# Kernel tuning notes

Hardware: AMD Instinct MI355X
Metric: run time of the kernel (lower is better)

## Reference

```python
import jax, jax.numpy as jnp
import numpy as np

E, K, H, I = 16, 4, 2048, 1024
B, S = 1, 2048


def setup_inputs() -> dict:
    key = jax.random.key(0)
    ks = jax.random.split(key, 5)
    scale_in = 1.0 / np.sqrt(H)
    scale_mid = 1.0 / np.sqrt(I)
    return {
        "x": jax.random.normal(ks[0], (B, S, H), dtype=jnp.float32),
        "gate_w": jax.random.normal(ks[1], (E, H), dtype=jnp.float32) * scale_in,
        "w1_gate": jax.random.normal(ks[2], (E, I, H), dtype=jnp.float32) * scale_in,
        "w1_up": jax.random.normal(ks[3], (E, I, H), dtype=jnp.float32) * scale_in,
        "w2": jax.random.normal(ks[4], (E, H, I), dtype=jnp.float32) * scale_mid,
        "topk": K,
    }


def reference(x, gate_w, w1_gate, w1_up, w2, topk):
    orig_shape = x.shape
    xt = x.reshape(-1, x.shape[-1])            # [T, H]
    T = xt.shape[0]
    n_exp = gate_w.shape[0]

    # Router: top-k logits, softmax over the selected k (as in the torch code).
    logits = xt @ gate_w.T                      # [T, E]
    topk_vals, topk_ids = jax.lax.top_k(logits, topk)
    topk_w = jax.nn.softmax(topk_vals, axis=-1)  # [T, K]

    # Dense per-token-per-expert combine weight; 0 for unselected experts.
    # Mathematically identical to the gather/scatter-add loop: unselected
    # experts contribute expert_out * 0.
    gate_dense = jnp.zeros((T, n_exp), dtype=xt.dtype)
    gate_dense = gate_dense.at[jnp.arange(T)[:, None], topk_ids].add(topk_w)

    # SwiGLU per expert (dense over experts; weights zero-out unused ones).
    g = jnp.einsum("th,eih->tei", xt, w1_gate)   # [T, E, I]
    u = jnp.einsum("th,eih->tei", xt, w1_up)     # [T, E, I]
    h = jax.nn.silu(g) * u                        # [T, E, I]
    out = jnp.einsum("tei,te,ehi->th", h, gate_dense, w2)  # [T, H]
    return out.reshape(orig_shape)
```

## Files before the change

### kernel.cpp

```cpp
#include <hip/hip_runtime.h>
#include <hip/hip_bf16.h>
#include <stdint.h>

#define NEXP 16
#define KSEL 4
#define HDIM 2048
#define IDIM 1024
#define TTOK 2048
#define MAXTILES 80
#define NTA 8
#define NTB 16
#define MAXBA (MAXTILES * NTA)
#define MAXBB (MAXTILES * NTB)

typedef __attribute__((ext_vector_type(8))) short bf16x8;
typedef __attribute__((ext_vector_type(4))) float f32x4;
typedef unsigned int u32;

__device__ __forceinline__ uint32_t pack2(float a, float b) {
  __hip_bfloat162 h = __float22bfloat162_rn(float2{a, b});
  uint32_t u;
  __builtin_memcpy(&u, &h, 4);
  return u;
}
__device__ __forceinline__ ushort bf1(float a) {
  __hip_bfloat16 h = __float2bfloat16(a);
  ushort u;
  __builtin_memcpy(&u, &h, 2);
  return u;
}
__device__ __forceinline__ float bf2f(ushort u) {
  uint32_t v = (uint32_t)u << 16;
  float f;
  __builtin_memcpy(&f, &v, 4);
  return f;
}
__device__ __forceinline__ void gload16(const ushort* g, ushort* l) {
  __builtin_amdgcn_global_load_lds(
      (const __attribute__((address_space(1))) u32*)g,
      (__attribute__((address_space(3))) u32*)l, 16, 0, 0);
}
__device__ __forceinline__ int swzread(int row, int q) {
  return row * 32 + ((q ^ ((row >> 1) & 3)) << 3);
}

__global__ __launch_bounds__(256) void cvtw_kernel(
    const float* __restrict__ src, ushort* __restrict__ dst, int n8)
{
  const int stride = gridDim.x * 256;
  for (int i = blockIdx.x * 256 + threadIdx.x; i < n8; i += stride) {
    float4 a = ((const float4*)src)[i * 2];
    float4 b = ((const float4*)src)[i * 2 + 1];
    uint4 t;
    t.x = pack2(a.x, a.y); t.y = pack2(a.z, a.w);
    t.z = pack2(b.x, b.y); t.w = pack2(b.z, b.w);
    ((uint4*)dst)[i] = t;
  }
}

__global__ __launch_bounds__(256) void router_kernel(
    const float* __restrict__ x, const float* __restrict__ gw,
    ushort* __restrict__ xb, int* __restrict__ topk_id,
    float* __restrict__ topk_w)
{
  const int wid = threadIdx.x >> 6;
  const int lane = threadIdx.x & 63;
  const int t = blockIdx.x * 4 + wid;
  const float4* x4 = (const float4*)(x + (size_t)t * HDIM);
  const float4* gw4 = (const float4*)gw;
  float acc[NEXP];
#pragma unroll
  for (int e = 0; e < NEXP; ++e) acc[e] = 0.f;
#pragma unroll
  for (int i = 0; i < HDIM / 256; ++i) {
    const int idx = i * 64 + lane;
    float4 xv = x4[idx];
    uint2 xp;
    xp.x = pack2(xv.x, xv.y);
    xp.y = pack2(xv.z, xv.w);
    *(uint2*)(xb + (size_t)t * HDIM + idx * 4) = xp;
#pragma unroll
    for (int e = 0; e < NEXP; ++e) {
      float4 wv = gw4[e * (HDIM / 4) + idx];
      acc[e] += xv.x * wv.x + xv.y * wv.y + xv.z * wv.z + xv.w * wv.w;
    }
  }
#pragma unroll
  for (int e = 0; e < NEXP; ++e) {
#pragma unroll
    for (int off = 32; off >= 1; off >>= 1)
      acc[e] += __shfl_xor(acc[e], off);
  }
  if (lane == 0) {
    unsigned taken = 0;
    float vals[KSEL];
    int ids[KSEL];
#pragma unroll
    for (int k = 0; k < KSEL; ++k) {
      float bv = -3.4e38f; int bi = 0;
      for (int e = 0; e < NEXP; ++e)
        if (!((taken >> e) & 1u) && acc[e] > bv) { bv = acc[e]; bi = e; }
      taken |= 1u << bi; vals[k] = bv; ids[k] = bi;
    }
    float m = vals[0], s = 0.f, w[KSEL];
#pragma unroll
    for (int k = 0; k < KSEL; ++k) { w[k] = __expf(vals[k] - m); s += w[k]; }
    float is = 1.f / s;
#pragma unroll
    for (int k = 0; k < KSEL; ++k) {
      topk_id[t * KSEL + k] = ids[k];
      topk_w[t * KSEL + k] = w[k] * is;
    }
  }
}

__global__ __launch_bounds__(1024) void plan_scatter_kernel(
    const int* __restrict__ topk_id, int* __restrict__ counts,
    int* __restrict__ offsets, int* __restrict__ nWA, int* __restrict__ nWB,
    int* __restrict__ wlA, int* __restrict__ wlB,
    int* __restrict__ rowTok, int* __restrict__ inv)
{
  __shared__ int cnt[NEXP], off[NEXP], cur[NEXP], tiles[NEXP], pre[NEXP];
  const int tid = threadIdx.x;
  if (tid < NEXP) { cnt[tid] = 0; cur[tid] = 0; }
  __syncthreads();
  for (int i = tid; i < TTOK * KSEL; i += 1024)
    atomicAdd(&cnt[topk_id[i]], 1);
  __syncthreads();
  if (tid == 0) {
    int s = 0, p = 0;
    for (int e = 0; e < NEXP; ++e) {
      off[e] = s; s += cnt[e];
      tiles[e] = (cnt[e] + 127) >> 7;
      pre[e] = p; p += tiles[e];
    }
    *nWA = p * NTA;
    *nWB = p * NTB;
  }
  __syncthreads();
  if (tid < NEXP) {
    counts[tid] = cnt[tid];
    offsets[tid] = off[tid];
    const int e = tid, T = tiles[e];
    int idx = pre[e] * NTA;
    for (int nt = 0; nt < NTA; ++nt)
      for (int mt = 0; mt < T; ++mt)
        wlA[idx++] = (e << 12) | (nt << 6) | mt;
  } else if (tid < 2 * NEXP) {
    const int e = tid - NEXP, T = tiles[e];
    int idx = pre[e] * NTB;
    for (int nt = 0; nt < NTB; ++nt)
      for (int mt = 0; mt < T; ++mt)
        wlB[idx++] = (e << 12) | (nt << 6) | mt;
  }
  for (int i = tid; i < TTOK * KSEL; i += 1024) {
    const int e = topk_id[i];
    const int pos = atomicAdd(&cur[e], 1);
    const int row = off[e] + pos;
    rowTok[row] = i >> 2;
    inv[i] = row;
  }
}

__global__ __launch_bounds__(256) void gemmA_kernel(
    const ushort* __restrict__ xb, const ushort* __restrict__ wb,
    const int* __restrict__ rowTok, const int* __restrict__ counts,
    const int* __restrict__ offsets, const int* __restrict__ nW,
    const int* __restrict__ wl, ushort* __restrict__ outb)
{
  const int nTot = *nW;
  const int L = (blockIdx.x & 7) * (MAXBA / 8) + (blockIdx.x >> 3);
  if (L >= nTot) return;
  const int w = wl[L];
  const int e = w >> 12, nt = (w >> 6) & 63, mt = w & 63;
  const int n_e = counts[e], rowbase = offsets[e];

  __shared__ ushort As[2][128 * 32];
  __shared__ ushort Bs[2][128 * 32];

  const int tid = threadIdx.x;
  const int r0 = tid >> 2;
  const int ck = tid & 3;
  const int sch = (ck ^ ((r0 >> 1) & 3)) << 3;

  const int ar0 = mt * 128 + r0, ar1 = ar0 + 64;
  const int tok0 = rowTok[rowbase + (ar0 < n_e ? ar0 : n_e - 1)];
  const int tok1 = rowTok[rowbase + (ar1 < n_e ? ar1 : n_e - 1)];
  const ushort* pA0 = xb + (size_t)tok0 * HDIM + sch;
  const ushort* pA1 = xb + (size_t)tok1 * HDIM + sch;
  const size_t wbase = (size_t)e * IDIM * HDIM;
  const ushort* pB0 = wb + wbase + (size_t)(nt * 128 + r0) * HDIM + sch;
  const ushort* pB1 = wb + wbase + (size_t)(nt * 128 + r0 + 64) * HDIM + sch;

  const int lane = tid & 63;
  const int wid = tid >> 6;
  const int wr = (wid >> 1) << 6;
  const int wc = (wid & 1) << 6;
  const int lr = lane & 15;
  const int q = lane >> 4;

  f32x4 acc[4][4];
#pragma unroll
  for (int i = 0; i < 4; ++i)
#pragma unroll
    for (int j = 0; j < 4; ++j) acc[i][j] = (f32x4){0.f, 0.f, 0.f, 0.f};

  auto STAGE = [&](int b) {
    gload16(pA0, &As[b][tid * 8]);
    gload16(pA1, &As[b][2048 + tid * 8]);
    gload16(pB0, &Bs[b][tid * 8]);
    gload16(pB1, &Bs[b][2048 + tid * 8]);
    pA0 += 32; pA1 += 32; pB0 += 32; pB1 += 32;
  };

  const int NTK = HDIM / 32;
  STAGE(0);
  __syncthreads();
  int buf = 0;
  for (int kt = 0; kt < NTK; ++kt) {
    if (kt + 1 < NTK) STAGE(buf ^ 1);
    bf16x8 af[4], bfr[4];
#pragma unroll
    for (int mi = 0; mi < 4; ++mi)
      af[mi] = *(const bf16x8*)&As[buf][swzread(wr + mi * 16 + lr, q)];
#pragma unroll
    for (int ni = 0; ni < 4; ++ni)
      bfr[ni] = *(const bf16x8*)&Bs[buf][swzread(wc + ni * 16 + lr, q)];
#pragma unroll
    for (int mi = 0; mi < 4; ++mi)
#pragma unroll
      for (int ni = 0; ni < 4; ++ni)
        acc[mi][ni] = __builtin_amdgcn_mfma_f32_16x16x32_bf16(af[mi], bfr[ni], acc[mi][ni], 0, 0, 0);
    __syncthreads();
    buf ^= 1;
  }

#pragma unroll
  for (int mi = 0; mi < 4; ++mi) {
#pragma unroll
    for (int ni = 0; ni < 4; ++ni) {
      const int col = nt * 128 + wc + ni * 16 + lr;
#pragma unroll
      for (int r = 0; r < 4; ++r) {
        const int mrow = mt * 128 + wr + mi * 16 + q * 4 + r;
        if (mrow < n_e)
          outb[(size_t)(rowbase + mrow) * IDIM + col] = bf1(acc[mi][ni][r]);
      }
    }
  }
}

__global__ __launch_bounds__(256) void gemmB_kernel(
    const ushort* __restrict__ hb, const ushort* __restrict__ wb,
    const int* __restrict__ counts, const int* __restrict__ offsets,
    const int* __restrict__ nW, const int* __restrict__ wl,
    ushort* __restrict__ po)
{
  const int nTot = *nW;
  const int L = (blockIdx.x & 7) * (MAXBB / 8) + (blockIdx.x >> 3);
  if (L >= nTot) return;
  const int w = wl[L];
  const int e = w >> 12, nt = (w >> 6) & 63, mt = w & 63;
  const int n_e = counts[e], rowbase = offsets[e];

  __shared__ ushort As[2][128 * 32];
  __shared__ ushort Bs[2][128 * 32];

  const int tid = threadIdx.x;
  const int r0 = tid >> 2;
  const int ck = tid & 3;
  const int sch = (ck ^ ((r0 >> 1) & 3)) << 3;

  const int ar0 = mt * 128 + r0, ar1 = ar0 + 64;
  const int g0 = rowbase + (ar0 < n_e ? ar0 : n_e - 1);
  const int g1 = rowbase + (ar1 < n_e ? ar1 : n_e - 1);
  const ushort* pA0 = hb + (size_t)g0 * IDIM + sch;
  const ushort* pA1 = hb + (size_t)g1 * IDIM + sch;
  const size_t wbase = (size_t)e * HDIM * IDIM;
  const ushort* pB0 = wb + wbase + (size_t)(nt * 128 + r0) * IDIM + sch;
  const ushort* pB1 = wb + wbase + (size_t)(nt * 128 + r0 + 64) * IDIM + sch;

  const int lane = tid & 63;
  const int wid = tid >> 6;
  const int wr = (wid >> 1) << 6;
  const int wc = (wid & 1) << 6;
  const int lr = lane & 15;
  const int q = lane >> 4;

  f32x4 acc[4][4];
#pragma unroll
  for (int i = 0; i < 4; ++i)
#pragma unroll
    for (int j = 0; j < 4; ++j) acc[i][j] = (f32x4){0.f, 0.f, 0.f, 0.f};

  auto STAGE = [&](int b) {
    gload16(pA0, &As[b][tid * 8]);
    gload16(pA1, &As[b][2048 + tid * 8]);
    gload16(pB0, &Bs[b][tid * 8]);
    gload16(pB1, &Bs[b][2048 + tid * 8]);
    pA0 += 32; pA1 += 32; pB0 += 32; pB1 += 32;
  };

  const int NTK = IDIM / 32;
  STAGE(0);
  __syncthreads();
  int buf = 0;
  for (int kt = 0; kt < NTK; ++kt) {
    if (kt + 1 < NTK) STAGE(buf ^ 1);
    bf16x8 af[4], bfr[4];
#pragma unroll
    for (int mi = 0; mi < 4; ++mi)
      af[mi] = *(const bf16x8*)&As[buf][swzread(wr + mi * 16 + lr, q)];
#pragma unroll
    for (int ni = 0; ni < 4; ++ni)
      bfr[ni] = *(const bf16x8*)&Bs[buf][swzread(wc + ni * 16 + lr, q)];
#pragma unroll
    for (int mi = 0; mi < 4; ++mi)
#pragma unroll
      for (int ni = 0; ni < 4; ++ni)
        acc[mi][ni] = __builtin_amdgcn_mfma_f32_16x16x32_bf16(af[mi], bfr[ni], acc[mi][ni], 0, 0, 0);
    __syncthreads();
    buf ^= 1;
  }

#pragma unroll
  for (int mi = 0; mi < 4; ++mi) {
#pragma unroll
    for (int ni = 0; ni < 4; ++ni) {
      const int col = nt * 128 + wc + ni * 16 + lr;
#pragma unroll
      for (int r = 0; r < 4; ++r) {
        const int mrow = mt * 128 + wr + mi * 16 + q * 4 + r;
        if (mrow < n_e)
          po[(size_t)(rowbase + mrow) * HDIM + col] = bf1(acc[mi][ni][r]);
      }
    }
  }
}

__global__ __launch_bounds__(256) void silu_kernel(
    const ushort* __restrict__ g, const ushort* __restrict__ u,
    ushort* __restrict__ h, int n8)
{
  const int stride = gridDim.x * 256;
  for (int i = blockIdx.x * 256 + threadIdx.x; i < n8; i += stride) {
    uint4 gv = ((const uint4*)g)[i];
    uint4 uv = ((const uint4*)u)[i];
    uint4 hv;
#pragma unroll
    for (int wd = 0; wd < 4; ++wd) {
      const uint32_t gw2 = (&gv.x)[wd], uw2 = (&uv.x)[wd];
      const float g0 = bf2f((ushort)(gw2 & 0xffff));
      const float g1 = bf2f((ushort)(gw2 >> 16));
      const float u0 = bf2f((ushort)(uw2 & 0xffff));
      const float u1 = bf2f((ushort)(uw2 >> 16));
      const float h0 = (g0 / (1.f + __expf(-g0))) * u0;
      const float h1 = (g1 / (1.f + __expf(-g1))) * u1;
      (&hv.x)[wd] = pack2(h0, h1);
    }
    ((uint4*)h)[i] = hv;
  }
}

__global__ __launch_bounds__(256) void combine_kernel(
    const ushort* __restrict__ po, const int* __restrict__ inv,
    const float* __restrict__ tw, float* __restrict__ out)
{
  const int t = blockIdx.x;
  const int r0 = inv[t * 4 + 0], r1 = inv[t * 4 + 1];
  const int r2 = inv[t * 4 + 2], r3 = inv[t * 4 + 3];
  const float w0 = tw[t * 4 + 0], w1 = tw[t * 4 + 1];
  const float w2v = tw[t * 4 + 2], w3 = tw[t * 4 + 3];
  const int i = threadIdx.x;
  uint4 v0 = *(const uint4*)(po + (size_t)r0 * HDIM + i * 8);
  uint4 v1 = *(const uint4*)(po + (size_t)r1 * HDIM + i * 8);
  uint4 v2 = *(const uint4*)(po + (size_t)r2 * HDIM + i * 8);
  uint4 v3 = *(const uint4*)(po + (size_t)r3 * HDIM + i * 8);
  float o[8];
#pragma unroll
  for (int w = 0; w < 4; ++w) {
    const uint32_t a = (&v0.x)[w], b = (&v1.x)[w], c = (&v2.x)[w], d = (&v3.x)[w];
    o[w * 2 + 0] = w0 * __builtin_bit_cast(float, a << 16) +
                   w1 * __builtin_bit_cast(float, b << 16) +
                   w2v * __builtin_bit_cast(float, c << 16) +
                   w3 * __builtin_bit_cast(float, d << 16);
    o[w * 2 + 1] = w0 * __builtin_bit_cast(float, a & 0xffff0000u) +
                   w1 * __builtin_bit_cast(float, b & 0xffff0000u) +
                   w2v * __builtin_bit_cast(float, c & 0xffff0000u) +
                   w3 * __builtin_bit_cast(float, d & 0xffff0000u);
  }
  float4* o4 = (float4*)(out + (size_t)t * HDIM + i * 8);
  o4[0] = (float4){o[0], o[1], o[2], o[3]};
  o4[1] = (float4){o[4], o[5], o[6], o[7]};
}

extern "C" void kernel_launch(void* const* d_in, const int* in_sizes, int n_in,
                              void* d_out, int out_size, void* d_ws, size_t ws_size,
                              hipStream_t stream) {
  const float* x   = (const float*)d_in[0];
  const float* gw  = (const float*)d_in[1];
  const float* w1g = (const float*)d_in[2];
  const float* w1u = (const float*)d_in[3];
  const float* w2  = (const float*)d_in[4];
  float* out = (float*)d_out;

  char* ws = (char*)d_ws;
  ushort* xb   = (ushort*)(ws + 0);
  ushort* wbuf = (ushort*)(ws + 8388608);
  ushort* gbuf = (ushort*)(ws + 75497472);
  ushort* ubuf = (ushort*)(ws + 92274688);
  ushort* hbuf = (ushort*)(ws + 109051904);
  ushort* po   = (ushort*)(ws + 125829120);
  int*    tkid   = (int*)(ws + 159383552);
  float*  tkw    = (float*)(ws + 159383552 + 32768);
  int*    rowTok = (int*)(ws + 159383552 + 65536);
  int*    inv    = (int*)(ws + 159383552 + 98304);
  int*    ctrl   = (int*)(ws + 159514624);
  int* counts  = ctrl;
  int* offsets = ctrl + 32;
  int* nWA     = ctrl + 50;
  int* nWB     = ctrl + 51;
  int* wlA     = ctrl + 64;
  int* wlB     = ctrl + 64 + MAXBA;

  const int NW8 = (NEXP * IDIM * HDIM) / 8;

  router_kernel<<<TTOK / 4, 256, 0, stream>>>(x, gw, xb, tkid, tkw);
  plan_scatter_kernel<<<1, 1024, 0, stream>>>(tkid, counts, offsets, nWA, nWB,
                                              wlA, wlB, rowTok, inv);
  cvtw_kernel<<<2048, 256, 0, stream>>>(w1g, wbuf, NW8);
  gemmA_kernel<<<MAXBA, 256, 0, stream>>>(xb, wbuf, rowTok, counts, offsets,
                                          nWA, wlA, gbuf);
  cvtw_kernel<<<2048, 256, 0, stream>>>(w1u, wbuf, NW8);
  gemmA_kernel<<<MAXBA, 256, 0, stream>>>(xb, wbuf, rowTok, counts, offsets,
                                          nWA, wlA, ubuf);
  silu_kernel<<<2048, 256, 0, stream>>>(gbuf, ubuf, hbuf, (TTOK * KSEL * IDIM) / 8);
  cvtw_kernel<<<2048, 256, 0, stream>>>(w2, wbuf, NW8);
  gemmB_kernel<<<MAXBB, 256, 0, stream>>>(hbuf, wbuf, counts, offsets,
                                          nWB, wlB, po);
  combine_kernel<<<TTOK, 256, 0, stream>>>(po, inv, tkw, out);
}
```

Measured before the change: 379.3 us.

## Fuse fp32-to-bf16 weight conversion into GEMM tile loads

Removes the three standalone weight conversion kernels and has the expert GEMMs stream fp32 weights straight into shared memory, converting to bf16 when fragments are read for MFMA. This avoids writing and re-reading bf16 copies of every weight tensor and shrinks the workspace. In exchange, the B tile in shared memory doubles in size, lowering occupancy. Each weight tile is now fetched at fp32 width by every token tile, and conversion ALU work is added in the inner loop.

```diff
diff --git a/kernel.cpp b/kernel.cpp
--- a/kernel.cpp
+++ b/kernel.cpp
@@ -35,27 +35,24 @@
   __builtin_memcpy(&f, &v, 4);
   return f;
 }
-__device__ __forceinline__ void gload16(const ushort* g, ushort* l) {
+__device__ __forceinline__ bf16x8 cvt8(const uint4& lo, const uint4& hi) {
+  float4 a, b;
+  __builtin_memcpy(&a, &lo, 16);
+  __builtin_memcpy(&b, &hi, 16);
+  uint4 t;
+  t.x = pack2(a.x, a.y); t.y = pack2(a.z, a.w);
+  t.z = pack2(b.x, b.y); t.w = pack2(b.z, b.w);
+  bf16x8 r;
+  __builtin_memcpy(&r, &t, 16);
+  return r;
+}
+__device__ __forceinline__ void gload16(const void* g, void* l) {
   __builtin_amdgcn_global_load_lds(
       (const __attribute__((address_space(1))) u32*)g,
       (__attribute__((address_space(3))) u32*)l, 16, 0, 0);
 }
 __device__ __forceinline__ int swzread(int row, int q) {
   return row * 32 + ((q ^ ((row >> 1) & 3)) << 3);
-}
-
-__global__ __launch_bounds__(256) void cvtw_kernel(
-    const float* __restrict__ src, ushort* __restrict__ dst, int n8)
-{
-  const int stride = gridDim.x * 256;
-  for (int i = blockIdx.x * 256 + threadIdx.x; i < n8; i += stride) {
-    float4 a = ((const float4*)src)[i * 2];
-    float4 b = ((const float4*)src)[i * 2 + 1];
-    uint4 t;
-    t.x = pack2(a.x, a.y); t.y = pack2(a.z, a.w);
-    t.z = pack2(b.x, b.y); t.w = pack2(b.z, b.w);
-    ((uint4*)dst)[i] = t;
-  }
 }
 
 __global__ __launch_bounds__(256) void router_kernel(
@@ -163,7 +160,7 @@
 }
 
 __global__ __launch_bounds__(256) void gemmA_kernel(
-    const ushort* __restrict__ xb, const ushort* __restrict__ wb,
+    const ushort* __restrict__ xb, const float* __restrict__ wsrc,
     const int* __restrict__ rowTok, const int* __restrict__ counts,
     const int* __restrict__ offsets, const int* __restrict__ nW,
     const int* __restrict__ wl, ushort* __restrict__ outb)
@@ -176,21 +173,25 @@
   const int n_e = counts[e], rowbase = offsets[e];
 
   __shared__ ushort As[2][128 * 32];
-  __shared__ ushort Bs[2][128 * 32];
+  __shared__ float  Bs[2][128 * 32];
 
   const int tid = threadIdx.x;
-  const int r0 = tid >> 2;
-  const int ck = tid & 3;
-  const int sch = (ck ^ ((r0 >> 1) & 3)) << 3;
-
-  const int ar0 = mt * 128 + r0, ar1 = ar0 + 64;
+  const int rA = tid >> 2;
+  const int ckA = tid & 3;
+  const int schA = (ckA ^ ((rA >> 1) & 3)) << 3;
+  const int ar0 = mt * 128 + rA, ar1 = ar0 + 64;
   const int tok0 = rowTok[rowbase + (ar0 < n_e ? ar0 : n_e - 1)];
   const int tok1 = rowTok[rowbase + (ar1 < n_e ? ar1 : n_e - 1)];
-  const ushort* pA0 = xb + (size_t)tok0 * HDIM + sch;
-  const ushort* pA1 = xb + (size_t)tok1 * HDIM + sch;
+  const ushort* pA0 = xb + (size_t)tok0 * HDIM + schA;
+  const ushort* pA1 = xb + (size_t)tok1 * HDIM + schA;
+  const int rB = tid >> 3;
+  const int ckB = tid & 7;
+  const int schB = (ckB ^ (rB & 7)) << 2;
+  const float* pB[4];
   const size_t wbase = (size_t)e * IDIM * HDIM;
-  const ushort* pB0 = wb + wbase + (size_t)(nt * 128 + r0) * HDIM + sch;
-  const ushort* pB1 = wb + wbase + (size_t)(nt * 128 + r0 + 64) * HDIM + sch;
+#pragma unroll
+  for (int c = 0; c < 4; ++c)
+    pB[c] = wsrc + wbase + (size_t)(nt * 128 + c * 32 + rB) * HDIM + schB;
 
   const int lane = tid & 63;
   const int wid = tid >> 6;
@@ -208,9 +209,12 @@
   auto STAGE = [&](int b) {
     gload16(pA0, &As[b][tid * 8]);
     gload16(pA1, &As[b][2048 + tid * 8]);
-    gload16(pB0, &Bs[b][tid * 8]);
-    gload16(pB1, &Bs[b][2048 + tid * 8]);
-    pA0 += 32; pA1 += 32; pB0 += 32; pB1 += 32;
+#pragma unroll
+    for (int c = 0; c < 4; ++c)
+      gload16(pB[c], &Bs[b][c * 1024 + tid * 4]);
+    pA0 += 32; pA1 += 32;
+#pragma unroll
+    for (int c = 0; c < 4; ++c) pB[c] += 32;
   };
 
   const int NTK = HDIM / 32;
@@ -224,8 +228,14 @@
     for (int mi = 0; mi < 4; ++mi)
       af[mi] = *(const bf16x8*)&As[buf][swzread(wr + mi * 16 + lr, q)];
 #pragma unroll
-    for (int ni = 0; ni < 4; ++ni)
-      bfr[ni] = *(const bf16x8*)&Bs[buf][swzread(wc + ni * 16 + lr, q)];
+    for (int ni = 0; ni < 4; ++ni) {
+      const int row = wc + ni * 16 + lr;
+      const int xr = row & 7;
+      const float* bp = &Bs[buf][row * 32];
+      uint4 lo = *(const uint4*)(bp + (((2 * q) ^ xr) << 2));
+      uint4 hi = *(const uint4*)(bp + (((2 * q + 1) ^ xr) << 2));
+      bfr[ni] = cvt8(lo, hi);
+    }
 #pragma unroll
     for (int mi = 0; mi < 4; ++mi)
 #pragma unroll
@@ -251,7 +261,7 @@
 }
 
 __global__ __launch_bounds__(256) void gemmB_kernel(
-    const ushort* __restrict__ hb, const ushort* __restrict__ wb,
+    const ushort* __restrict__ hb, const float* __restrict__ wsrc,
     const int* __restrict__ counts, const int* __restrict__ offsets,
     const int* __restrict__ nW, const int* __restrict__ wl,
     ushort* __restrict__ po)
@@ -264,21 +274,25 @@
   const int n_e = counts[e], rowbase = offsets[e];
 
   __shared__ ushort As[2][128 * 32];
-  __shared__ ushort Bs[2][128 * 32];
+  __shared__ float  Bs[2][128 * 32];
 
   const int tid = threadIdx.x;
-  const int r0 = tid >> 2;
-  const int ck = tid & 3;
-  const int sch = (ck ^ ((r0 >> 1) & 3)) << 3;
-
-  const int ar0 = mt * 128 + r0, ar1 = ar0 + 64;
+  const int rA = tid >> 2;
+  const int ckA = tid & 3;
+  const int schA = (ckA ^ ((rA >> 1) & 3)) << 3;
+  const int ar0 = mt * 128 + rA, ar1 = ar0 + 64;
   const int g0 = rowbase + (ar0 < n_e ? ar0 : n_e - 1);
   const int g1 = rowbase + (ar1 < n_e ? ar1 : n_e - 1);
-  const ushort* pA0 = hb + (size_t)g0 * IDIM + sch;
-  const ushort* pA1 = hb + (size_t)g1 * IDIM + sch;
+  const ushort* pA0 = hb + (size_t)g0 * IDIM + schA;
+  const ushort* pA1 = hb + (size_t)g1 * IDIM + schA;
+  const int rB = tid >> 3;
+  const int ckB = tid & 7;
+  const int schB = (ckB ^ (rB & 7)) << 2;
+  const float* pB[4];
   const size_t wbase = (size_t)e * HDIM * IDIM;
-  const ushort* pB0 = wb + wbase + (size_t)(nt * 128 + r0) * IDIM + sch;
-  const ushort* pB1 = wb + wbase + (size_t)(nt * 128 + r0 + 64) * IDIM + sch;
+#pragma unroll
+  for (int c = 0; c < 4; ++c)
+    pB[c] = wsrc + wbase + (size_t)(nt * 128 + c * 32 + rB) * IDIM + schB;
 
   const int lane = tid & 63;
   const int wid = tid >> 6;
@@ -296,9 +310,12 @@
   auto STAGE = [&](int b) {
     gload16(pA0, &As[b][tid * 8]);
     gload16(pA1, &As[b][2048 + tid * 8]);
-    gload16(pB0, &Bs[b][tid * 8]);
-    gload16(pB1, &Bs[b][2048 + tid * 8]);
-    pA0 += 32; pA1 += 32; pB0 += 32; pB1 += 32;
+#pragma unroll
+    for (int c = 0; c < 4; ++c)
+      gload16(pB[c], &Bs[b][c * 1024 + tid * 4]);
+    pA0 += 32; pA1 += 32;
+#pragma unroll
+    for (int c = 0; c < 4; ++c) pB[c] += 32;
   };
 
   const int NTK = IDIM / 32;
@@ -312,8 +329,14 @@
     for (int mi = 0; mi < 4; ++mi)
       af[mi] = *(const bf16x8*)&As[buf][swzread(wr + mi * 16 + lr, q)];
 #pragma unroll
-    for (int ni = 0; ni < 4; ++ni)
-      bfr[ni] = *(const bf16x8*)&Bs[buf][swzread(wc + ni * 16 + lr, q)];
+    for (int ni = 0; ni < 4; ++ni) {
+      const int row = wc + ni * 16 + lr;
+      const int xr = row & 7;
+      const float* bp = &Bs[buf][row * 32];
+      uint4 lo = *(const uint4*)(bp + (((2 * q) ^ xr) << 2));
+      uint4 hi = *(const uint4*)(bp + (((2 * q + 1) ^ xr) << 2));
+      bfr[ni] = cvt8(lo, hi);
+    }
 #pragma unroll
     for (int mi = 0; mi < 4; ++mi)
 #pragma unroll
@@ -406,16 +429,15 @@
 
   char* ws = (char*)d_ws;
   ushort* xb   = (ushort*)(ws + 0);
-  ushort* wbuf = (ushort*)(ws + 8388608);
-  ushort* gbuf = (ushort*)(ws + 75497472);
-  ushort* ubuf = (ushort*)(ws + 92274688);
-  ushort* hbuf = (ushort*)(ws + 109051904);
-  ushort* po   = (ushort*)(ws + 125829120);
-  int*    tkid   = (int*)(ws + 159383552);
-  float*  tkw    = (float*)(ws + 159383552 + 32768);
-  int*    rowTok = (int*)(ws + 159383552 + 65536);
-  int*    inv    = (int*)(ws + 159383552 + 98304);
-  int*    ctrl   = (int*)(ws + 159514624);
+  ushort* gbuf = (ushort*)(ws + 8388608);
+  ushort* ubuf = (ushort*)(ws + 25165824);
+  ushort* hbuf = (ushort*)(ws + 41943040);
+  ushort* po   = (ushort*)(ws + 58720256);
+  int*    tkid   = (int*)(ws + 92274688);
+  float*  tkw    = (float*)(ws + 92274688 + 32768);
+  int*    rowTok = (int*)(ws + 92274688 + 65536);
+  int*    inv    = (int*)(ws + 92274688 + 98304);
+  int*    ctrl   = (int*)(ws + 92405760);
   int* counts  = ctrl;
   int* offsets = ctrl + 32;
   int* nWA     = ctrl + 50;
@@ -423,20 +445,15 @@
   int* wlA     = ctrl + 64;
   int* wlB     = ctrl + 64 + MAXBA;
 
-  const int NW8 = (NEXP * IDIM * HDIM) / 8;
-
   router_kernel<<<TTOK / 4, 256, 0, stream>>>(x, gw, xb, tkid, tkw);
   plan_scatter_kernel<<<1, 1024, 0, stream>>>(tkid, counts, offsets, nWA, nWB,
                                               wlA, wlB, rowTok, inv);
-  cvtw_kernel<<<2048, 256, 0, stream>>>(w1g, wbuf, NW8);
-  gemmA_kernel<<<MAXBA, 256, 0, stream>>>(xb, wbuf, rowTok, counts, offsets,
+  gemmA_kernel<<<MAXBA, 256, 0, stream>>>(xb, w1g, rowTok, counts, offsets,
                                           nWA, wlA, gbuf);
-  cvtw_kernel<<<2048, 256, 0, stream>>>(w1u, wbuf, NW8);
-  gemmA_kernel<<<MAXBA, 256, 0, stream>>>(xb, wbuf, rowTok, counts, offsets,
+  gemmA_kernel<<<MAXBA, 256, 0, stream>>>(xb, w1u, rowTok, counts, offsets,
                                           nWA, wlA, ubuf);
   silu_kernel<<<2048, 256, 0, stream>>>(gbuf, ubuf, hbuf, (TTOK * KSEL * IDIM) / 8);
-  cvtw_kernel<<<2048, 256, 0, stream>>>(w2, wbuf, NW8);
-  gemmB_kernel<<<MAXBB, 256, 0, stream>>>(hbuf, wbuf, counts, offsets,
+  gemmB_kernel<<<MAXBB, 256, 0, stream>>>(hbuf, w2, counts, offsets,
                                           nWB, wlB, po);
   combine_kernel<<<TTOK, 256, 0, stream>>>(po, inv, tkw, out);
 }
```

Result: slower. 470.7 us (+24.1%).

## Fuse gate and up GEMMs with SiLU epilogue and merge weight conversions

Applied to the files above, without the earlier changes.

Gate and up projections now run in one GEMM kernel that shares the A-tile loads, keeps two accumulator sets, and applies SiLU*up in the epilogue. This removes the separate silu kernel, the g/u intermediate buffers and one pass of A loads. The gate and up weight conversions are also merged into one kernel. In exchange, accumulator registers and LDS per block double (to 48KB LDS), which may lower occupancy, and the po buffer now aliases the wU region.

```diff
diff --git a/kernel.cpp b/kernel.cpp
--- a/kernel.cpp
+++ b/kernel.cpp
@@ -35,27 +35,13 @@
   __builtin_memcpy(&f, &v, 4);
   return f;
 }
-__device__ __forceinline__ void gload16(const ushort* g, ushort* l) {
+__device__ __forceinline__ void gload16(const void* g, void* l) {
   __builtin_amdgcn_global_load_lds(
       (const __attribute__((address_space(1))) u32*)g,
       (__attribute__((address_space(3))) u32*)l, 16, 0, 0);
 }
 __device__ __forceinline__ int swzread(int row, int q) {
   return row * 32 + ((q ^ ((row >> 1) & 3)) << 3);
-}
-
-__global__ __launch_bounds__(256) void cvtw_kernel(
-    const float* __restrict__ src, ushort* __restrict__ dst, int n8)
-{
-  const int stride = gridDim.x * 256;
-  for (int i = blockIdx.x * 256 + threadIdx.x; i < n8; i += stride) {
-    float4 a = ((const float4*)src)[i * 2];
-    float4 b = ((const float4*)src)[i * 2 + 1];
-    uint4 t;
-    t.x = pack2(a.x, a.y); t.y = pack2(a.z, a.w);
-    t.z = pack2(b.x, b.y); t.w = pack2(b.z, b.w);
-    ((uint4*)dst)[i] = t;
-  }
 }
 
 __global__ __launch_bounds__(256) void router_kernel(
@@ -162,11 +148,46 @@
   }
 }
 
-__global__ __launch_bounds__(256) void gemmA_kernel(
-    const ushort* __restrict__ xb, const ushort* __restrict__ wb,
-    const int* __restrict__ rowTok, const int* __restrict__ counts,
-    const int* __restrict__ offsets, const int* __restrict__ nW,
-    const int* __restrict__ wl, ushort* __restrict__ outb)
+__global__ __launch_bounds__(256) void cvtGU_kernel(
+    const float* __restrict__ srcG, const float* __restrict__ srcU,
+    ushort* __restrict__ dstG, ushort* __restrict__ dstU, int n8)
+{
+  const int stride = gridDim.x * 256;
+  for (int i = blockIdx.x * 256 + threadIdx.x; i < n8; i += stride) {
+    float4 a = ((const float4*)srcG)[i * 2];
+    float4 b = ((const float4*)srcG)[i * 2 + 1];
+    uint4 t;
+    t.x = pack2(a.x, a.y); t.y = pack2(a.z, a.w);
+    t.z = pack2(b.x, b.y); t.w = pack2(b.z, b.w);
+    ((uint4*)dstG)[i] = t;
+    a = ((const float4*)srcU)[i * 2];
+    b = ((const float4*)srcU)[i * 2 + 1];
+    t.x = pack2(a.x, a.y); t.y = pack2(a.z, a.w);
+    t.z = pack2(b.x, b.y); t.w = pack2(b.z, b.w);
+    ((uint4*)dstU)[i] = t;
+  }
+}
+
+__global__ __launch_bounds__(256) void cvtw_kernel(
+    const float* __restrict__ src, ushort* __restrict__ dst, int n8)
+{
+  const int stride = gridDim.x * 256;
+  for (int i = blockIdx.x * 256 + threadIdx.x; i < n8; i += stride) {
+    float4 a = ((const float4*)src)[i * 2];
+    float4 b = ((const float4*)src)[i * 2 + 1];
+    uint4 t;
+    t.x = pack2(a.x, a.y); t.y = pack2(a.z, a.w);
+    t.z = pack2(b.x, b.y); t.w = pack2(b.z, b.w);
+    ((uint4*)dst)[i] = t;
+  }
+}
+
+__global__ __launch_bounds__(256) void gemm1_kernel(
+    const ushort* __restrict__ xb, const ushort* __restrict__ wg,
+    const ushort* __restrict__ wu, const int* __restrict__ rowTok,
+    const int* __restrict__ counts, const int* __restrict__ offsets,
+    const int* __restrict__ nW, const int* __restrict__ wl,
+    ushort* __restrict__ hbuf)
 {
   const int nTot = *nW;
   const int L = (blockIdx.x & 7) * (MAXBA / 8) + (blockIdx.x >> 3);
@@ -176,7 +197,8 @@
   const int n_e = counts[e], rowbase = offsets[e];
 
   __shared__ ushort As[2][128 * 32];
-  __shared__ ushort Bs[2][128 * 32];
+  __shared__ ushort Bg[2][128 * 32];
+  __shared__ ushort Bu[2][128 * 32];
 
   const int tid = threadIdx.x;
   const int r0 = tid >> 2;
@@ -189,8 +211,10 @@
   const ushort* pA0 = xb + (size_t)tok0 * HDIM + sch;
   const ushort* pA1 = xb + (size_t)tok1 * HDIM + sch;
   const size_t wbase = (size_t)e * IDIM * HDIM;
-  const ushort* pB0 = wb + wbase + (size_t)(nt * 128 + r0) * HDIM + sch;
-  const ushort* pB1 = wb + wbase + (size_t)(nt * 128 + r0 + 64) * HDIM + sch;
+  const ushort* pG0 = wg + wbase + (size_t)(nt * 128 + r0) * HDIM + sch;
+  const ushort* pG1 = wg + wbase + (size_t)(nt * 128 + r0 + 64) * HDIM + sch;
+  const ushort* pU0 = wu + wbase + (size_t)(nt * 128 + r0) * HDIM + sch;
+  const ushort* pU1 = wu + wbase + (size_t)(nt * 128 + r0 + 64) * HDIM + sch;
 
   const int lane = tid & 63;
   const int wid = tid >> 6;
@@ -199,18 +223,23 @@
   const int lr = lane & 15;
   const int q = lane >> 4;
 
-  f32x4 acc[4][4];
+  f32x4 accG[4][4], accU[4][4];
 #pragma unroll
   for (int i = 0; i < 4; ++i)
 #pragma unroll
-    for (int j = 0; j < 4; ++j) acc[i][j] = (f32x4){0.f, 0.f, 0.f, 0.f};
+    for (int j = 0; j < 4; ++j) {
+      accG[i][j] = (f32x4){0.f, 0.f, 0.f, 0.f};
+      accU[i][j] = (f32x4){0.f, 0.f, 0.f, 0.f};
+    }
 
   auto STAGE = [&](int b) {
     gload16(pA0, &As[b][tid * 8]);
     gload16(pA1, &As[b][2048 + tid * 8]);
-    gload16(pB0, &Bs[b][tid * 8]);
-    gload16(pB1, &Bs[b][2048 + tid * 8]);
-    pA0 += 32; pA1 += 32; pB0 += 32; pB1 += 32;
+    gload16(pG0, &Bg[b][tid * 8]);
+    gload16(pG1, &Bg[b][2048 + tid * 8]);
+    gload16(pU0, &Bu[b][tid * 8]);
+    gload16(pU1, &Bu[b][2048 + tid * 8]);
+    pA0 += 32; pA1 += 32; pG0 += 32; pG1 += 32; pU0 += 32; pU1 += 32;
   };
 
   const int NTK = HDIM / 32;
@@ -219,18 +248,22 @@
   int buf = 0;
   for (int kt = 0; kt < NTK; ++kt) {
     if (kt + 1 < NTK) STAGE(buf ^ 1);
-    bf16x8 af[4], bfr[4];
+    bf16x8 af[4], bg[4], bu[4];
 #pragma unroll
     for (int mi = 0; mi < 4; ++mi)
       af[mi] = *(const bf16x8*)&As[buf][swzread(wr + mi * 16 + lr, q)];
 #pragma unroll
-    for (int ni = 0; ni < 4; ++ni)
-      bfr[ni] = *(const bf16x8*)&Bs[buf][swzread(wc + ni * 16 + lr, q)];
+    for (int ni = 0; ni < 4; ++ni) {
+      bg[ni] = *(const bf16x8*)&Bg[buf][swzread(wc + ni * 16 + lr, q)];
+      bu[ni] = *(const bf16x8*)&Bu[buf][swzread(wc + ni * 16 + lr, q)];
+    }
 #pragma unroll
     for (int mi = 0; mi < 4; ++mi)
 #pragma unroll
-      for (int ni = 0; ni < 4; ++ni)
-        acc[mi][ni] = __builtin_amdgcn_mfma_f32_16x16x32_bf16(af[mi], bfr[ni], acc[mi][ni], 0, 0, 0);
+      for (int ni = 0; ni < 4; ++ni) {
+        accG[mi][ni] = __builtin_amdgcn_mfma_f32_16x16x32_bf16(af[mi], bg[ni], accG[mi][ni], 0, 0, 0);
+        accU[mi][ni] = __builtin_amdgcn_mfma_f32_16x16x32_bf16(af[mi], bu[ni], accU[mi][ni], 0, 0, 0);
+      }
     __syncthreads();
     buf ^= 1;
   }
@@ -243,8 +276,12 @@
 #pragma unroll
       for (int r = 0; r < 4; ++r) {
         const int mrow = mt * 128 + wr + mi * 16 + q * 4 + r;
-        if (mrow < n_e)
-          outb[(size_t)(rowbase + mrow) * IDIM + col] = bf1(acc[mi][ni][r]);
+        if (mrow < n_e) {
+          const float gv = accG[mi][ni][r];
+          const float uv = accU[mi][ni][r];
+          const float hv = (gv / (1.f + __expf(-gv))) * uv;
+          hbuf[(size_t)(rowbase + mrow) * IDIM + col] = bf1(hv);
+        }
       }
     }
   }
@@ -335,30 +372,6 @@
           po[(size_t)(rowbase + mrow) * HDIM + col] = bf1(acc[mi][ni][r]);
       }
     }
-  }
-}
-
-__global__ __launch_bounds__(256) void silu_kernel(
-    const ushort* __restrict__ g, const ushort* __restrict__ u,
-    ushort* __restrict__ h, int n8)
-{
-  const int stride = gridDim.x * 256;
-  for (int i = blockIdx.x * 256 + threadIdx.x; i < n8; i += stride) {
-    uint4 gv = ((const uint4*)g)[i];
-    uint4 uv = ((const uint4*)u)[i];
-    uint4 hv;
-#pragma unroll
-    for (int wd = 0; wd < 4; ++wd) {
-      const uint32_t gw2 = (&gv.x)[wd], uw2 = (&uv.x)[wd];
-      const float g0 = bf2f((ushort)(gw2 & 0xffff));
-      const float g1 = bf2f((ushort)(gw2 >> 16));
-      const float u0 = bf2f((ushort)(uw2 & 0xffff));
-      const float u1 = bf2f((ushort)(uw2 >> 16));
-      const float h0 = (g0 / (1.f + __expf(-g0))) * u0;
-      const float h1 = (g1 / (1.f + __expf(-g1))) * u1;
-      (&hv.x)[wd] = pack2(h0, h1);
-    }
-    ((uint4*)h)[i] = hv;
   }
 }
 
@@ -406,11 +419,10 @@
 
   char* ws = (char*)d_ws;
   ushort* xb   = (ushort*)(ws + 0);
-  ushort* wbuf = (ushort*)(ws + 8388608);
-  ushort* gbuf = (ushort*)(ws + 75497472);
-  ushort* ubuf = (ushort*)(ws + 92274688);
-  ushort* hbuf = (ushort*)(ws + 109051904);
-  ushort* po   = (ushort*)(ws + 125829120);
+  ushort* wG   = (ushort*)(ws + 8388608);
+  ushort* wU   = (ushort*)(ws + 75497472);
+  ushort* po   = (ushort*)(ws + 75497472);
+  ushort* hbuf = (ushort*)(ws + 142606336);
   int*    tkid   = (int*)(ws + 159383552);
   float*  tkw    = (float*)(ws + 159383552 + 32768);
   int*    rowTok = (int*)(ws + 159383552 + 65536);
@@ -428,15 +440,11 @@
   router_kernel<<<TTOK / 4, 256, 0, stream>>>(x, gw, xb, tkid, tkw);
   plan_scatter_kernel<<<1, 1024, 0, stream>>>(tkid, counts, offsets, nWA, nWB,
                                               wlA, wlB, rowTok, inv);
-  cvtw_kernel<<<2048, 256, 0, stream>>>(w1g, wbuf, NW8);
-  gemmA_kernel<<<MAXBA, 256, 0, stream>>>(xb, wbuf, rowTok, counts, offsets,
-                                          nWA, wlA, gbuf);
-  cvtw_kernel<<<2048, 256, 0, stream>>>(w1u, wbuf, NW8);
-  gemmA_kernel<<<MAXBA, 256, 0, stream>>>(xb, wbuf, rowTok, counts, offsets,
-                                          nWA, wlA, ubuf);
-  silu_kernel<<<2048, 256, 0, stream>>>(gbuf, ubuf, hbuf, (TTOK * KSEL * IDIM) / 8);
-  cvtw_kernel<<<2048, 256, 0, stream>>>(w2, wbuf, NW8);
-  gemmB_kernel<<<MAXBB, 256, 0, stream>>>(hbuf, wbuf, counts, offsets,
+  cvtGU_kernel<<<2048, 256, 0, stream>>>(w1g, w1u, wG, wU, NW8);
+  gemm1_kernel<<<MAXBA, 256, 0, stream>>>(xb, wG, wU, rowTok, counts, offsets,
+                                          nWA, wlA, hbuf);
+  cvtw_kernel<<<2048, 256, 0, stream>>>(w2, wG, NW8);
+  gemmB_kernel<<<MAXBB, 256, 0, stream>>>(hbuf, wG, counts, offsets,
                                           nWB, wlB, po);
   combine_kernel<<<TTOK, 256, 0, stream>>>(po, inv, tkw, out);
 }
```

Result: slower. 476.9 us (+25.7%).
